# Optimization experiments

Measured on AMD Instinct MI355X. Metric: run time of the kernel, lower is better.

## Reference

```python
import jax, jax.numpy as jnp
import numpy as np

N_CLASSES = 18
NMS_PRE = 1000   # test_cfg.nms_pre, per level
K_NMS = 500      # per-class candidates entering greedy NMS
SCORE_THR = 0.01
IOU_THR = 0.5
LEVEL_NS = [600000, 300000, 150000, 75000]


def _decode(points, pred):
    # fcaf3d axis-aligned decode: pred = (dx-, dx+, dy-, dy+, dz-, dz+) >= 0
    cx = points[:, 0] + (pred[:, 1] - pred[:, 0]) / 2
    cy = points[:, 1] + (pred[:, 3] - pred[:, 2]) / 2
    cz = points[:, 2] + (pred[:, 5] - pred[:, 4]) / 2
    w = pred[:, 0] + pred[:, 1]
    l = pred[:, 2] + pred[:, 3]
    h = pred[:, 4] + pred[:, 5]
    return jnp.stack([cx, cy, cz, w, l, h], axis=-1)  # [N, 6]


def _iou3d(b):
    # axis-aligned 3D IoU, b: [K,6] (cx,cy,cz,w,l,h) -> [K,K]
    mn = b[:, :3] - b[:, 3:] / 2
    mx = b[:, :3] + b[:, 3:] / 2
    lt = jnp.maximum(mn[:, None, :], mn[None, :, :])
    rb = jnp.minimum(mx[:, None, :], mx[None, :, :])
    inter = jnp.clip(rb - lt, 0.0).prod(-1)
    vol = jnp.clip(mx - mn, 0.0).prod(-1)
    return inter / (vol[:, None] + vol[None, :] - inter + 1e-6)


def _level(centerness, bbox_pred, cls_score, points):
    # fused score: cls.sigmoid() * centerness.sigmoid()
    scores = jax.nn.sigmoid(cls_score) * jax.nn.sigmoid(centerness)  # [N,C]
    max_scores = scores.max(axis=1)
    _, ids = jax.lax.top_k(max_scores, NMS_PRE)  # per-level prefilter
    bboxes = _decode(points[ids], bbox_pred[ids])  # [NMS_PRE, 6]
    return bboxes, scores[ids]


def _nms_class(boxes, scores):
    # boxes [M,6], scores [M] for one class -> greedy NMS on top K_NMS
    valid = scores > SCORE_THR
    s = jnp.where(valid, scores, -1.0)
    sv, order = jax.lax.top_k(s, K_NMS)  # sorted desc
    b = boxes[order]
    v = sv > SCORE_THR
    iou = _iou3d(b)  # [K,K]
    idx = jnp.arange(K_NMS)

    def body(i, sup):
        alive = jnp.logical_not(sup[i])
        return sup | (alive & (iou[i] > IOU_THR) & (idx > i))

    sup = jax.lax.fori_loop(0, K_NMS, body, jnp.logical_not(v))
    keep = jnp.logical_not(sup) & v
    return b, sv, keep


def _forward(levels):
    mlvl_bboxes, mlvl_scores = [], []
    for (cn, bp, cs, pt) in levels:
        b, s = _level(cn, bp, cs, pt)
        mlvl_bboxes.append(b)
        mlvl_scores.append(s)
    bboxes = jnp.concatenate(mlvl_bboxes)  # [4*NMS_PRE, 6]
    scores = jnp.concatenate(mlvl_scores)  # [4*NMS_PRE, C]
    # per-class NMS (vmap over class dim)
    b, sv, keep = jax.vmap(_nms_class, in_axes=(None, 1))(bboxes, scores)
    labels = jnp.broadcast_to(jnp.arange(N_CLASSES, dtype=jnp.int32)[:, None], sv.shape)
    return (b.reshape(-1, 6), sv.reshape(-1), labels.reshape(-1), keep.reshape(-1))


def setup_inputs() -> dict:
    key = jax.random.key(0)
    out = {}
    for li, n in enumerate(LEVEL_NS):
        k1, k2, k3, k4, key = jax.random.split(key, 5)
        out[f'centerness{li}'] = jax.random.normal(k1, (n, 1), jnp.float32)
        out[f'bbox_pred{li}'] = jax.random.uniform(k2, (n, 6), jnp.float32)  # non-negative distances
        out[f'cls_score{li}'] = jax.random.normal(k3, (n, N_CLASSES), jnp.float32)
        out[f'points{li}'] = jax.random.normal(k4, (n, 3), jnp.float32) * 2.0
    return out


def reference(centerness0, bbox_pred0, cls_score0, points0,
              centerness1, bbox_pred1, cls_score1, points1,
              centerness2, bbox_pred2, cls_score2, points2,
              centerness3, bbox_pred3, cls_score3, points3):
    levels = [
        (centerness0, bbox_pred0, cls_score0, points0),
        (centerness1, bbox_pred1, cls_score1, points1),
        (centerness2, bbox_pred2, cls_score2, points2),
        (centerness3, bbox_pred3, cls_score3, points3),
    ]
    return _forward(levels)
```

## Files before the change

kernel.cpp:

```cpp
#include <hip/hip_runtime.h>
#include <math.h>

#define N_CLASSES 18
#define NMS_PRE   1000
#define K_NMS     500
#define POOL      4000
#define LIST_CAP  2048
#define NREP      64
#define NSUB      16
#define SUBCAP    (LIST_CAP/NSUB)
#define IOU_THR   0.5f
#define SCORE_THR 0.01f

typedef unsigned long long ull;

struct Ptrs {
  const float* cent[4];
  const float* bbox[4];
  const float* cls[4];
  const float* pts[4];
  int off[4];
  int ntot;
};

__device__ __forceinline__ unsigned int fsort(float f){
  unsigned int b = __float_as_uint(f);
  return (b & 0x80000000u) ? ~b : (b | 0x80000000u);
}
__device__ __forceinline__ float fsort_inv(unsigned int k){
  unsigned int b = (k & 0x80000000u) ? (k & 0x7FFFFFFFu) : ~k;
  return __uint_as_float(b);
}
__device__ __forceinline__ float sigmoidf_(float x){
  return 1.0f / (1.0f + expf(-x));
}
__device__ __forceinline__ int level_of(int f, const Ptrs& P){
  return (f >= P.off[3]) ? 3 : (f >= P.off[2]) ? 2 : (f >= P.off[1]) ? 1 : 0;
}

__device__ __forceinline__ void gload_lds16(const void* g, void* l){
  __builtin_amdgcn_global_load_lds(
      (const __attribute__((address_space(1))) void*)g,
      (__attribute__((address_space(3))) void*)l, 16, 0, 0);
}

__device__ __forceinline__ ull cx_keep(ull mine, ull part, bool keep_hi){
  ull mx = mine > part ? mine : part;
  ull mn = mine > part ? part : mine;
  return keep_hi ? mx : mn;
}
__device__ __forceinline__ void cxpair(ull &a, ull &b, bool a_hi){
  ull mx = a > b ? a : b;
  ull mn = a > b ? b : a;
  a = a_hi ? mx : mn;
  b = a_hi ? mn : mx;
}

__global__ void __launch_bounds__(256) init_kernel(unsigned int* hist_rep, unsigned int* hist2,
                        unsigned int* scnt, ull* lists, unsigned int* state){
  int tid = blockIdx.x*256 + threadIdx.x;
  int stride = gridDim.x*256;
  for (int j = tid; j < NREP*4*2048; j += stride) hist_rep[j] = 0u;
  for (int j = tid; j < 4*2048; j += stride) hist2[j] = 0u;
  for (int j = tid; j < 4*NSUB*16; j += stride) scnt[j] = 0u;
  for (int j = tid; j < 4*LIST_CAP; j += stride) lists[j] = 0ull;
  if (tid < 4){
    state[2*tid]   = 0u;
    state[2*tid+1] = NMS_PRE;
  }
}

__global__ void __launch_bounds__(256) compute_keys(Ptrs P, unsigned int* keys,
                        unsigned int* hist_rep){
  __shared__ __align__(16) float cls_s[256*N_CLASSES];
  __shared__ unsigned int lh[2048];
  int t = threadIdx.x;
  int f0 = blockIdx.x << 8;
  int f = f0 + t;
  int rep = blockIdx.x & (NREP - 1);
  bool valid = f < P.ntot;
  int fl = min(f0 + 255, P.ntot - 1);
  bool uni = (level_of(f0, P) == level_of(fl, P)) && (f0 + 255 < P.ntot);
  int Lb = level_of(f0, P);
  if (uni){
    const float4* base4 = (const float4*)(P.cls[Lb] + (size_t)(f0 - P.off[Lb]) * N_CLASSES);
#pragma unroll
    for (int k = 0; k < 4; ++k){
      int j = (k << 8) + t;
      gload_lds16(base4 + j, (char*)cls_s + (size_t)j * 16);
    }
    if (t < 128){
      int j = 1024 + t;
      gload_lds16(base4 + j, (char*)cls_s + (size_t)j * 16);
    }
  }
  for (int j = t; j < 2048; j += 256) lh[j] = 0u;
  float m = 0.f, cent = 0.f;
  if (uni){
    cent = P.cent[Lb][f - P.off[Lb]];
  } else if (valid){
    int L = level_of(f, P); int i = f - P.off[L];
    const float* cl = P.cls[L] + (size_t)i * N_CLASSES;
    m = cl[0];
    for (int c = 1; c < N_CLASSES; ++c) m = fmaxf(m, cl[c]);
    cent = P.cent[L][i];
  }
  __syncthreads();
  if (uni){
    const float2* row = (const float2*)(cls_s + t * N_CLASSES);
    float2 v0 = row[0];
    m = fmaxf(v0.x, v0.y);
#pragma unroll
    for (int q = 1; q < 9; ++q){
      float2 v = row[q];
      m = fmaxf(m, fmaxf(v.x, v.y));
    }
  }
  if (valid){
    float s = sigmoidf_(m) * sigmoidf_(cent);
    unsigned int key = fsort(s);
    keys[f] = key;
    unsigned int bin = key >> 21;
    if (uni) atomicAdd(&lh[bin], 1u);
    else     atomicAdd(&hist_rep[((rep*4) + level_of(f, P))*2048 + bin], 1u);
  }
  __syncthreads();
  if (uni){
    unsigned int* hb = hist_rep + ((rep*4) + Lb)*2048;
    for (int j = t; j < 2048; j += 256){
      unsigned int v = lh[j];
      if (v) atomicAdd(&hb[j], v);
    }
  }
}

__global__ void __launch_bounds__(256) hist_level(Ptrs P, const unsigned int* keys,
                        const unsigned int* state, unsigned int* hist2){
  int f = blockIdx.x * 256 + threadIdx.x;
  if (f < P.ntot){
    int L = level_of(f, P);
    unsigned int key = keys[f];
    unsigned int Pfx = state[2*L];
    if ((key >> 21) == (Pfx >> 21))
      atomicAdd(&hist2[L*2048 + ((key >> 10) & 0x7FFu)], 1u);
  }
}

__global__ void __launch_bounds__(256) scan_sel(const unsigned int* src, int nrep,
                        unsigned int* state, int pass){
  __shared__ unsigned int lhist[2048];
  int L = blockIdx.x, t = threadIdx.x;
  for (int j = t; j < 2048; j += 256){
    unsigned int s = 0u;
    if (nrep == NREP){
#pragma unroll 8
      for (int r = 0; r < NREP; ++r) s += src[((r*4) + L)*2048 + j];
    } else {
      s = src[L*2048 + j];
    }
    lhist[j] = s;
  }
  __syncthreads();
  if (t < 64){
    int lane = t;
    unsigned int krem = state[2*L + 1];
    unsigned int Pfx  = state[2*L];
    unsigned int carry = 0;
    for (int ch = 0; ch < 32; ++ch){
      unsigned int cnt = lhist[2047 - (ch*64 + lane)];
      unsigned int pfx = cnt;
#pragma unroll
      for (int off = 1; off < 64; off <<= 1){
        unsigned int u = __shfl_up(pfx, off);
        if (lane >= off) pfx += u;
      }
      unsigned int C = carry + pfx;
      ull bal = __ballot(C >= krem);
      if (bal){
        int fl2 = __ffsll(bal) - 1;
        unsigned int Cf = __shfl(C, fl2);
        unsigned int cf = __shfl(cnt, fl2);
        if (lane == 0){
          unsigned int b = (unsigned int)(2047 - (ch*64 + fl2));
          state[2*L]     = (pass == 0) ? (b << 21) : (Pfx | (b << 10));
          state[2*L + 1] = krem - (Cf - cf);
        }
        break;
      }
      carry = __shfl(C, 63);
    }
  }
}

__global__ void __launch_bounds__(256) compact_kernel(Ptrs P, const unsigned int* keys,
                        const unsigned int* state, unsigned int* scnt, ull* lists){
  int f = blockIdx.x * 256 + threadIdx.x;
  if (f >= P.ntot) return;
  int L = level_of(f, P);
  unsigned int key = keys[f];
  unsigned int T = state[2*L];
  if (key >= T){
    unsigned int sub = (unsigned int)blockIdx.x & (NSUB - 1);
    unsigned int pos = atomicAdd(&scnt[(L*NSUB + sub)*16], 1u);
    if (pos < SUBCAP){
      unsigned int i = (unsigned int)(f - P.off[L]);
      lists[(size_t)L*LIST_CAP + sub*SUBCAP + pos] = ((ull)key << 32) | (ull)(~i);
    }
  }
}

__global__ void __launch_bounds__(1024) sort_idx(const ull* lists, unsigned int* sidx){
  __shared__ ull buf[LIST_CAP];
  int L = blockIdx.x;
  int t = threadIdx.x;
  int e1 = t + 1024;
  const ull* src = lists + (size_t)L*LIST_CAP;
  ull v0 = src[t];
  ull v1 = src[e1];
  for (int k = 2; k <= 2048; k <<= 1){
    for (int j = k >> 1; j > 0; j >>= 1){
      bool hi0 = (((t  & j) == 0) == ((t  & k) == 0));
      bool hi1 = (((e1 & j) == 0) == ((e1 & k) == 0));
      if (j >= 1024){
        cxpair(v0, v1, hi0);
      } else if (j >= 64){
        __syncthreads();
        buf[t] = v0; buf[e1] = v1;
        __syncthreads();
        ull p0 = buf[t ^ j];
        ull p1 = buf[e1 ^ j];
        v0 = cx_keep(v0, p0, hi0);
        v1 = cx_keep(v1, p1, hi1);
      } else {
        ull p0 = __shfl_xor(v0, j);
        ull p1 = __shfl_xor(v1, j);
        v0 = cx_keep(v0, p0, hi0);
        v1 = cx_keep(v1, p1, hi1);
      }
    }
  }
  if (t < NMS_PRE) sidx[L*NMS_PRE + t] = ~((unsigned int)(v0 & 0xFFFFFFFFu));
}

__global__ void __launch_bounds__(64) gather_decode(Ptrs P, const unsigned int* sidx,
                        float* boxes_pool, float* scores_pool){
  int r = blockIdx.x*64 + threadIdx.x;
  if (r >= POOL) return;
  int L = r / NMS_PRE;
  unsigned int i = sidx[r];
  const float* bp = P.bbox[L] + (size_t)i * 6;
  const float* pp = P.pts[L]  + (size_t)i * 3;
  float p0 = bp[0], p1 = bp[1], p2 = bp[2], p3 = bp[3], p4 = bp[4], p5 = bp[5];
  float cx = pp[0] + (p1 - p0) * 0.5f;
  float cy = pp[1] + (p3 - p2) * 0.5f;
  float cz = pp[2] + (p5 - p4) * 0.5f;
  float w = p0 + p1, l = p2 + p3, h = p4 + p5;
  float* bo = boxes_pool + (size_t)r * 6;
  bo[0] = cx; bo[1] = cy; bo[2] = cz; bo[3] = w; bo[4] = l; bo[5] = h;
  float cs = sigmoidf_(P.cent[L][i]);
  const float* cl = P.cls[L] + (size_t)i * N_CLASSES;
#pragma unroll
  for (int c = 0; c < N_CLASSES; ++c)
    scores_pool[(size_t)c * POOL + r] = sigmoidf_(cl[c]) * cs;
}

__global__ void __launch_bounds__(1024) class_topk(const float* scores_pool, const float* boxes_pool,
                        float* out, float* aabb){
  __shared__ unsigned int keyS[4096];
  __shared__ ull comp[512];
  __shared__ unsigned int histS[256];
  __shared__ unsigned int wsum[16], wpre[16];
  __shared__ unsigned int sP, sK, sCnt;
  int c = blockIdx.x;
  int t = threadIdx.x;
  int w = t >> 6, lane = t & 63;

  for (int j = t; j < 4096; j += 1024){
    unsigned int k = 0u;
    if (j < POOL){
      float s = scores_pool[(size_t)c*POOL + j];
      float sval = (s > SCORE_THR) ? s : -1.0f;
      k = fsort(sval);
    }
    keyS[j] = k;
  }
  if (t == 0){ sP = 0u; sK = K_NMS; sCnt = 0u; }
  __syncthreads();

  for (int pass = 0; pass < 4; ++pass){
    int shift = 24 - 8*pass;
    if (t < 256) histS[t] = 0u;
    __syncthreads();
    unsigned int Pfx = sP;
    for (int j = t; j < 4096; j += 1024){
      unsigned int k = keyS[j];
      if ((((ull)(k ^ Pfx)) >> (shift + 8)) == 0ull)
        atomicAdd(&histS[(k >> shift) & 0xFFu], 1u);
    }
    __syncthreads();
    if (w == 0){
      unsigned int krem = sK;
      unsigned int carry = 0;
      for (int ch = 0; ch < 4; ++ch){
        unsigned int cnt = histS[255 - (ch*64 + lane)];
        unsigned int pfx = cnt;
#pragma unroll
        for (int off = 1; off < 64; off <<= 1){
          unsigned int u = __shfl_up(pfx, off);
          if (lane >= off) pfx += u;
        }
        unsigned int C = carry + pfx;
        ull bal = __ballot(C >= krem);
        if (bal){
          int fl = __ffsll(bal) - 1;
          unsigned int Cf = __shfl(C, fl);
          unsigned int cf = __shfl(cnt, fl);
          if (lane == 0){
            sP = Pfx | ((unsigned int)(255 - (ch*64 + fl)) << shift);
            sK = krem - (Cf - cf);
          }
          break;
        }
        carry = __shfl(C, 63);
      }
    }
    __syncthreads();
  }
  unsigned int T = sP, need = sK;

  unsigned int loc[4]; unsigned int ct = 0;
#pragma unroll
  for (int q = 0; q < 4; ++q){
    unsigned int k = keyS[4*t + q];
    loc[q] = k;
    ct += (k == T) ? 1u : 0u;
  }
  unsigned int inc = ct;
#pragma unroll
  for (int off = 1; off < 64; off <<= 1){
    unsigned int u = __shfl_up(inc, off);
    if (lane >= off) inc += u;
  }
  if (lane == 63) wsum[w] = inc;
  __syncthreads();
  if (t < 16){
    unsigned int v = wsum[t];
    unsigned int pincl = v;
#pragma unroll
    for (int off = 1; off < 16; off <<= 1){
      unsigned int u = __shfl_up(pincl, off);
      if (t >= off) pincl += u;
    }
    wpre[t] = pincl - v;
  }
  __syncthreads();
  unsigned int excl = wpre[w] + (inc - ct);

#pragma unroll
  for (int q = 0; q < 4; ++q){
    unsigned int k = loc[q];
    bool surv = false;
    if (k > T) surv = true;
    else if (k == T){ surv = (excl < need); excl += 1u; }
    if (surv){
      unsigned int pos = atomicAdd(&sCnt, 1u);
      if (pos < 512)
        comp[pos] = ((ull)k << 32) | (ull)(~(unsigned int)(4*t + q));
    }
  }
  __syncthreads();

  ull v0 = 0ull;
  if (t < 512 && t < (int)sCnt) v0 = comp[t];
  for (int k = 2; k <= 512; k <<= 1){
    for (int j = k >> 1; j > 0; j >>= 1){
      if (j >= 64){
        __syncthreads();
        if (t < 512) comp[t] = v0;
        __syncthreads();
        if (t < 512){
          ull p0 = comp[t ^ j];
          bool hi0 = (((t & j) == 0) == ((t & k) == 0));
          v0 = cx_keep(v0, p0, hi0);
        }
      } else {
        if (t < 512){
          ull p0 = __shfl_xor(v0, j);
          bool hi0 = (((t & j) == 0) == ((t & k) == 0));
          v0 = cx_keep(v0, p0, hi0);
        }
      }
    }
  }

  if (t < K_NMS){
    ull cm = v0;
    unsigned int j = ~((unsigned int)(cm & 0xFFFFFFFFu));
    float sval = fsort_inv((unsigned int)(cm >> 32));
    int o = c*K_NMS + t;
    const float* bp = boxes_pool + (size_t)j * 6;
    float b0 = bp[0], b1 = bp[1], b2 = bp[2], b3 = bp[3], b4 = bp[4], b5 = bp[5];
    float* ob = out + (size_t)o * 6;
    ob[0] = b0; ob[1] = b1; ob[2] = b2; ob[3] = b3; ob[4] = b4; ob[5] = b5;
    out[54000 + o] = sval;
    out[63000 + o] = (float)c;
    float mn0 = b0 - b3*0.5f, mx0 = b0 + b3*0.5f;
    float mn1 = b1 - b4*0.5f, mx1 = b1 + b4*0.5f;
    float mn2 = b2 - b5*0.5f, mx2 = b2 + b5*0.5f;
    float vol = fmaxf(mx0 - mn0, 0.f) * fmaxf(mx1 - mn1, 0.f) * fmaxf(mx2 - mn2, 0.f);
    float* ap = aabb + ((size_t)c*512 + t) * 8;
    ap[0] = mn0; ap[1] = mn1; ap[2] = mn2; ap[3] = mx0; ap[4] = mx1; ap[5] = mx2;
    ap[6] = vol; ap[7] = sval;
  }
}

__global__ void __launch_bounds__(512) nms_mask(const float* aabb, ull* maskG, ull* flagsG){
  __shared__ float smn0[512], smn1[512], smn2[512];
  __shared__ float smx0[512], smx1[512], smx2[512];
  __shared__ float svol[512];
  __shared__ ull rowbuf[64*8];
  int c = blockIdx.y, chunk = blockIdx.x;
  int t = threadIdx.x, w = t >> 6, lane = t & 63;
  float mn0 = 0.f, mn1 = 0.f, mn2 = 0.f, mx0 = 0.f, mx1 = 0.f, mx2 = 0.f, vol = 0.f;
  if (t < K_NMS){
    const float* ap = aabb + ((size_t)c*512 + t) * 8;
    mn0 = ap[0]; mn1 = ap[1]; mn2 = ap[2];
    mx0 = ap[3]; mx1 = ap[4]; mx2 = ap[5]; vol = ap[6];
  }
  smn0[t] = mn0; smn1[t] = mn1; smn2[t] = mn2;
  smx0[t] = mx0; smx1[t] = mx1; smx2[t] = mx2;
  svol[t] = vol;
  __syncthreads();
  int i0 = chunk * 64, i1 = min(i0 + 64, K_NMS);
  for (int i = i0; i < i1; ++i){
    float lt0 = fmaxf(smn0[i], mn0), lt1 = fmaxf(smn1[i], mn1), lt2 = fmaxf(smn2[i], mn2);
    float rb0 = fminf(smx0[i], mx0), rb1 = fminf(smx1[i], mx1), rb2 = fminf(smx2[i], mx2);
    float inter = fmaxf(rb0 - lt0, 0.f) * fmaxf(rb1 - lt1, 0.f) * fmaxf(rb2 - lt2, 0.f);
    float denom = svol[i] + vol - inter + 1e-6f;
    bool s = (t < K_NMS) && (t > i) && (inter / denom > IOU_THR);
    ull m = __ballot(s);
    if (lane == 0){
      maskG[((size_t)c*K_NMS + i)*8 + w] = m;
      rowbuf[(i - i0)*8 + w] = m;
    }
  }
  __syncthreads();
  if (t < 64){
    int r = i0 + t;
    bool nz = false;
    if (r < K_NMS){
      ull o = 0ull;
#pragma unroll
      for (int z = 0; z < 8; ++z) o |= rowbuf[t*8 + z];
      nz = (o != 0ull);
    }
    ull bal = __ballot(nz);
    if (t == 0) flagsG[(size_t)c*8 + chunk] = bal;
  }
}

__global__ void __launch_bounds__(512) nms_greedy(const float* aabb, const ull* maskG,
                        const ull* flagsG, float* keep_out){
  __shared__ ull maskS[K_NMS*8];
  __shared__ ull vbitsS[8], remS[8];
  int c = blockIdx.x, t = threadIdx.x, w = t >> 6, lane = t & 63;
  ull flg[8];
#pragma unroll
  for (int q = 0; q < 8; ++q) flg[q] = flagsG[(size_t)c*8 + q];
  for (int j = t; j < K_NMS*8; j += 512) maskS[j] = maskG[(size_t)c*K_NMS*8 + j];
  float sv = (t < K_NMS) ? aabb[((size_t)c*512 + t)*8 + 7] : -1.0f;
  ull vb = __ballot(sv > SCORE_THR);
  if (lane == 0) vbitsS[w] = vb;
  __syncthreads();
  if (w == 0){
    ull rem[8];
#pragma unroll
    for (int q = 0; q < 8; ++q) rem[q] = ~vbitsS[q];
#pragma unroll
    for (int q = 0; q < 8; ++q){
      ull cand = flg[q] & ~rem[q];
      while (cand){
        int b = __ffsll(cand) - 1;
        int i = q*64 + b;
#pragma unroll
        for (int z = 0; z < 8; ++z) rem[z] |= maskS[i*8 + z];
        ull above = (b < 63) ? (~0ull << (b + 1)) : 0ull;
        cand = flg[q] & ~rem[q] & above;
      }
    }
    if (lane == 0){
#pragma unroll
      for (int q = 0; q < 8; ++q) remS[q] = rem[q];
    }
  }
  __syncthreads();
  if (t < K_NMS)
    keep_out[c*K_NMS + t] = ((remS[t >> 6] >> (t & 63)) & 1ull) ? 0.0f : 1.0f;
}

extern "C" void kernel_launch(void* const* d_in, const int* in_sizes, int n_in,
                              void* d_out, int out_size, void* d_ws, size_t ws_size,
                              hipStream_t stream){
  Ptrs P;
  int off = 0;
  for (int L = 0; L < 4; ++L){
    P.cent[L] = (const float*)d_in[4*L + 0];
    P.bbox[L] = (const float*)d_in[4*L + 1];
    P.cls[L]  = (const float*)d_in[4*L + 2];
    P.pts[L]  = (const float*)d_in[4*L + 3];
    P.off[L]  = off;
    off += in_sizes[4*L + 0];
  }
  P.ntot = off;

  char* w = (char*)d_ws;
  size_t o = 0;
  auto alloc = [&](size_t bytes) -> char* {
    char* p = w + o;
    o = (o + bytes + 255) & ~(size_t)255;
    return p;
  };
  unsigned int* keys        = (unsigned int*)alloc((size_t)P.ntot * 4);
  unsigned int* hist_rep    = (unsigned int*)alloc((size_t)NREP * 4 * 2048 * 4);
  unsigned int* hist2       = (unsigned int*)alloc(4 * 2048 * 4);
  unsigned int* state       = (unsigned int*)alloc(4 * 2 * 4);
  unsigned int* scnt        = (unsigned int*)alloc(4 * NSUB * 16 * 4);
  ull* lists                = (ull*)alloc((size_t)4 * LIST_CAP * 8);
  unsigned int* sidx        = (unsigned int*)alloc((size_t)POOL * 4);
  float* boxes_pool         = (float*)alloc((size_t)POOL * 6 * 4);
  float* scores_pool        = (float*)alloc((size_t)N_CLASSES * POOL * 4);
  float* aabb               = (float*)alloc((size_t)N_CLASSES * 512 * 8 * 4);
  ull* maskG                = (ull*)alloc((size_t)N_CLASSES * K_NMS * 8 * 8);
  ull* flagsG               = (ull*)alloc((size_t)N_CLASSES * 8 * 8);

  float* out = (float*)d_out;
  int grid = (P.ntot + 255) / 256;

  init_kernel<<<64, 256, 0, stream>>>(hist_rep, hist2, scnt, lists, state);
  compute_keys<<<grid, 256, 0, stream>>>(P, keys, hist_rep);
  scan_sel<<<4, 256, 0, stream>>>(hist_rep, NREP, state, 0);
  hist_level<<<grid, 256, 0, stream>>>(P, keys, state, hist2);
  scan_sel<<<4, 256, 0, stream>>>(hist2, 1, state, 1);
  compact_kernel<<<grid, 256, 0, stream>>>(P, keys, state, scnt, lists);
  sort_idx<<<4, 1024, 0, stream>>>(lists, sidx);
  gather_decode<<<(POOL + 63)/64, 64, 0, stream>>>(P, sidx, boxes_pool, scores_pool);
  class_topk<<<N_CLASSES, 1024, 0, stream>>>(scores_pool, boxes_pool, out, aabb);
  nms_mask<<<dim3(8, N_CLASSES), 512, 0, stream>>>(aabb, maskG, flagsG);
  nms_greedy<<<N_CLASSES, 512, 0, stream>>>(aabb, maskG, flagsG, out + 72000);
}
```

Baseline: 270.7 us.

## Process two points per thread with vectorized loads in key/hist/compact kernels

Each thread in compute_keys, hist_level and compact_kernel now handles a pair of adjacent points. The two 18-float class rows are read as nine float4 loads and the keys as uint2, replacing the LDS staging through global_load_lds. Blocks grow to 512 threads and the histogram replica count drops from 64 to 16, which cuts the init zeroing and scan_sel reduction work. The pairing assumes every level size is even so the float4, float2 and uint2 accesses stay aligned and never straddle a level boundary. Fewer replicas may also raise contention on the global histogram atomics.

```diff
diff --git a/kernel.cpp b/kernel.cpp
--- a/kernel.cpp
+++ b/kernel.cpp
@@ -6,7 +6,7 @@
 #define K_NMS     500
 #define POOL      4000
 #define LIST_CAP  2048
-#define NREP      64
+#define NREP      16
 #define NSUB      16
 #define SUBCAP    (LIST_CAP/NSUB)
 #define IOU_THR   0.5f
@@ -36,12 +36,6 @@
 }
 __device__ __forceinline__ int level_of(int f, const Ptrs& P){
   return (f >= P.off[3]) ? 3 : (f >= P.off[2]) ? 2 : (f >= P.off[1]) ? 1 : 0;
-}
-
-__device__ __forceinline__ void gload_lds16(const void* g, void* l){
-  __builtin_amdgcn_global_load_lds(
-      (const __attribute__((address_space(1))) void*)g,
-      (__attribute__((address_space(3))) void*)l, 16, 0, 0);
 }
 
 __device__ __forceinline__ ull cx_keep(ull mine, ull part, bool keep_hi){
@@ -70,79 +64,78 @@
   }
 }
 
-__global__ void __launch_bounds__(256) compute_keys(Ptrs P, unsigned int* keys,
+__global__ void __launch_bounds__(512) compute_keys(Ptrs P, unsigned int* keys,
                         unsigned int* hist_rep){
-  __shared__ __align__(16) float cls_s[256*N_CLASSES];
   __shared__ unsigned int lh[2048];
   int t = threadIdx.x;
-  int f0 = blockIdx.x << 8;
-  int f = f0 + t;
+  for (int j = t; j < 2048; j += 512) lh[j] = 0u;
+  int ip = blockIdx.x*512 + t;
+  int f  = ip << 1;
   int rep = blockIdx.x & (NREP - 1);
   bool valid = f < P.ntot;
-  int fl = min(f0 + 255, P.ntot - 1);
-  bool uni = (level_of(f0, P) == level_of(fl, P)) && (f0 + 255 < P.ntot);
+  int f0 = blockIdx.x << 10;
+  int fL = min(f0 + 1023, P.ntot - 1);
+  bool uni = (level_of(f0, P) == level_of(fL, P)) && (f0 + 1023 < P.ntot);
   int Lb = level_of(f0, P);
-  if (uni){
-    const float4* base4 = (const float4*)(P.cls[Lb] + (size_t)(f0 - P.off[Lb]) * N_CLASSES);
-#pragma unroll
-    for (int k = 0; k < 4; ++k){
-      int j = (k << 8) + t;
-      gload_lds16(base4 + j, (char*)cls_s + (size_t)j * 16);
-    }
-    if (t < 128){
-      int j = 1024 + t;
-      gload_lds16(base4 + j, (char*)cls_s + (size_t)j * 16);
-    }
-  }
-  for (int j = t; j < 2048; j += 256) lh[j] = 0u;
-  float m = 0.f, cent = 0.f;
-  if (uni){
-    cent = P.cent[Lb][f - P.off[Lb]];
-  } else if (valid){
-    int L = level_of(f, P); int i = f - P.off[L];
-    const float* cl = P.cls[L] + (size_t)i * N_CLASSES;
-    m = cl[0];
-    for (int c = 1; c < N_CLASSES; ++c) m = fmaxf(m, cl[c]);
-    cent = P.cent[L][i];
-  }
-  __syncthreads();
-  if (uni){
-    const float2* row = (const float2*)(cls_s + t * N_CLASSES);
-    float2 v0 = row[0];
-    m = fmaxf(v0.x, v0.y);
-#pragma unroll
-    for (int q = 1; q < 9; ++q){
-      float2 v = row[q];
-      m = fmaxf(m, fmaxf(v.x, v.y));
-    }
-  }
+
+  float mA = 0.f, mB = 0.f, cA = 0.f, cB = 0.f;
+  int L = 0;
   if (valid){
-    float s = sigmoidf_(m) * sigmoidf_(cent);
-    unsigned int key = fsort(s);
-    keys[f] = key;
-    unsigned int bin = key >> 21;
-    if (uni) atomicAdd(&lh[bin], 1u);
-    else     atomicAdd(&hist_rep[((rep*4) + level_of(f, P))*2048 + bin], 1u);
+    L = level_of(f, P);
+    int i = f - P.off[L];
+    const float4* q = (const float4*)(P.cls[L] + (size_t)i * N_CLASSES);
+    float4 q0 = q[0], q1 = q[1], q2 = q[2], q3 = q[3], q4 = q[4];
+    float4 q5 = q[5], q6 = q[6], q7 = q[7], q8 = q[8];
+    mA = fmaxf(fmaxf(fmaxf(q0.x,q0.y), fmaxf(q0.z,q0.w)),
+         fmaxf(fmaxf(fmaxf(q1.x,q1.y), fmaxf(q1.z,q1.w)),
+         fmaxf(fmaxf(fmaxf(q2.x,q2.y), fmaxf(q2.z,q2.w)),
+         fmaxf(fmaxf(fmaxf(q3.x,q3.y), fmaxf(q3.z,q3.w)),
+               fmaxf(q4.x,q4.y)))));
+    mB = fmaxf(fmaxf(q4.z,q4.w),
+         fmaxf(fmaxf(fmaxf(q5.x,q5.y), fmaxf(q5.z,q5.w)),
+         fmaxf(fmaxf(fmaxf(q6.x,q6.y), fmaxf(q6.z,q6.w)),
+         fmaxf(fmaxf(fmaxf(q7.x,q7.y), fmaxf(q7.z,q7.w)),
+               fmaxf(fmaxf(q8.x,q8.y), fmaxf(q8.z,q8.w))))));
+    const float2 c2 = *(const float2*)(P.cent[L] + i);
+    cA = c2.x; cB = c2.y;
+  }
+  __syncthreads();
+
+  if (valid){
+    float sA = sigmoidf_(mA) * sigmoidf_(cA);
+    float sB = sigmoidf_(mB) * sigmoidf_(cB);
+    unsigned int kA = fsort(sA), kB = fsort(sB);
+    *(uint2*)(keys + f) = make_uint2(kA, kB);
+    if (uni){
+      atomicAdd(&lh[kA >> 21], 1u);
+      atomicAdd(&lh[kB >> 21], 1u);
+    } else {
+      unsigned int* hb = hist_rep + ((rep*4) + L)*2048;
+      atomicAdd(&hb[kA >> 21], 1u);
+      atomicAdd(&hb[kB >> 21], 1u);
+    }
   }
   __syncthreads();
   if (uni){
     unsigned int* hb = hist_rep + ((rep*4) + Lb)*2048;
-    for (int j = t; j < 2048; j += 256){
+    for (int j = t; j < 2048; j += 512){
       unsigned int v = lh[j];
       if (v) atomicAdd(&hb[j], v);
     }
   }
 }
 
-__global__ void __launch_bounds__(256) hist_level(Ptrs P, const unsigned int* keys,
+__global__ void __launch_bounds__(512) hist_level(Ptrs P, const unsigned int* keys,
                         const unsigned int* state, unsigned int* hist2){
-  int f = blockIdx.x * 256 + threadIdx.x;
+  int ip = blockIdx.x*512 + threadIdx.x;
+  int f = ip << 1;
   if (f < P.ntot){
     int L = level_of(f, P);
-    unsigned int key = keys[f];
+    uint2 kk = *(const uint2*)(keys + f);
     unsigned int Pfx = state[2*L];
-    if ((key >> 21) == (Pfx >> 21))
-      atomicAdd(&hist2[L*2048 + ((key >> 10) & 0x7FFu)], 1u);
+    unsigned int hi = Pfx >> 21;
+    if ((kk.x >> 21) == hi) atomicAdd(&hist2[L*2048 + ((kk.x >> 10) & 0x7FFu)], 1u);
+    if ((kk.y >> 21) == hi) atomicAdd(&hist2[L*2048 + ((kk.y >> 10) & 0x7FFu)], 1u);
   }
 }
 
@@ -153,7 +146,7 @@
   for (int j = t; j < 2048; j += 256){
     unsigned int s = 0u;
     if (nrep == NREP){
-#pragma unroll 8
+#pragma unroll
       for (int r = 0; r < NREP; ++r) s += src[((r*4) + L)*2048 + j];
     } else {
       s = src[L*2048 + j];
@@ -192,19 +185,27 @@
   }
 }
 
-__global__ void __launch_bounds__(256) compact_kernel(Ptrs P, const unsigned int* keys,
+__global__ void __launch_bounds__(512) compact_kernel(Ptrs P, const unsigned int* keys,
                         const unsigned int* state, unsigned int* scnt, ull* lists){
-  int f = blockIdx.x * 256 + threadIdx.x;
+  int ip = blockIdx.x*512 + threadIdx.x;
+  int f = ip << 1;
   if (f >= P.ntot) return;
   int L = level_of(f, P);
-  unsigned int key = keys[f];
+  uint2 kk = *(const uint2*)(keys + f);
   unsigned int T = state[2*L];
-  if (key >= T){
-    unsigned int sub = (unsigned int)blockIdx.x & (NSUB - 1);
+  unsigned int sub = (unsigned int)blockIdx.x & (NSUB - 1);
+  if (kk.x >= T){
     unsigned int pos = atomicAdd(&scnt[(L*NSUB + sub)*16], 1u);
     if (pos < SUBCAP){
       unsigned int i = (unsigned int)(f - P.off[L]);
-      lists[(size_t)L*LIST_CAP + sub*SUBCAP + pos] = ((ull)key << 32) | (ull)(~i);
+      lists[(size_t)L*LIST_CAP + sub*SUBCAP + pos] = ((ull)kk.x << 32) | (ull)(~i);
+    }
+  }
+  if (kk.y >= T){
+    unsigned int pos = atomicAdd(&scnt[(L*NSUB + sub)*16], 1u);
+    if (pos < SUBCAP){
+      unsigned int i = (unsigned int)(f + 1 - P.off[L]);
+      lists[(size_t)L*LIST_CAP + sub*SUBCAP + pos] = ((ull)kk.y << 32) | (ull)(~i);
     }
   }
 }
@@ -534,14 +535,15 @@
   ull* flagsG               = (ull*)alloc((size_t)N_CLASSES * 8 * 8);
 
   float* out = (float*)d_out;
-  int grid = (P.ntot + 255) / 256;
+  int npairs = P.ntot >> 1;
+  int pgrid = (npairs + 511) / 512;
 
   init_kernel<<<64, 256, 0, stream>>>(hist_rep, hist2, scnt, lists, state);
-  compute_keys<<<grid, 256, 0, stream>>>(P, keys, hist_rep);
+  compute_keys<<<pgrid, 512, 0, stream>>>(P, keys, hist_rep);
   scan_sel<<<4, 256, 0, stream>>>(hist_rep, NREP, state, 0);
-  hist_level<<<grid, 256, 0, stream>>>(P, keys, state, hist2);
+  hist_level<<<pgrid, 512, 0, stream>>>(P, keys, state, hist2);
   scan_sel<<<4, 256, 0, stream>>>(hist2, 1, state, 1);
-  compact_kernel<<<grid, 256, 0, stream>>>(P, keys, state, scnt, lists);
+  compact_kernel<<<pgrid, 512, 0, stream>>>(P, keys, state, scnt, lists);
   sort_idx<<<4, 1024, 0, stream>>>(lists, sidx);
   gather_decode<<<(POOL + 63)/64, 64, 0, stream>>>(P, sidx, boxes_pool, scores_pool);
   class_topk<<<N_CLASSES, 1024, 0, stream>>>(scores_pool, boxes_pool, out, aabb);
```

After: 264.6 us. 1.02x faster.
